# Optimization experiments

Hardware: AMD Instinct MI355X
Metric: run time of the kernel (lower is better)

Reference implementation:

```python
import jax, jax.numpy as jnp
import numpy as np

# Module constants from init_kwargs
A, T, HID, H, EGO = 50, 50, 128, 32, 0
C = 4 * HID // H   # per-head out channels = 16
B = 32
NEG_SLOPE = 0.2    # PyG GATConv default negative_slope


def setup_inputs() -> dict:
    key = jax.random.key(0)
    k1, k2, k3, k4 = jax.random.split(key, 4)
    h = jax.random.normal(k1, (B, A, T, HID), dtype=jnp.float32)
    # GATConv params: lin.weight (H*C, HID), att_src/att_dst (H, C), bias (H*C,)
    W = jax.random.normal(k2, (H * C, HID), dtype=jnp.float32) * (1.0 / np.sqrt(HID))
    att_src = jax.random.normal(k3, (H, C), dtype=jnp.float32) * 0.1
    att_dst = jax.random.normal(k4, (H, C), dtype=jnp.float32) * 0.1
    bias = jnp.zeros((H * C,), dtype=jnp.float32)
    return {"h": h, "W": W, "att_src": att_src, "att_dst": att_dst, "bias": bias}


def reference(h, W, att_src, att_dst, bias):
    # h: (B, A, T, HID). Node id = t*A + a after permute, matching build_ego_star_edges.
    b = h.shape[0]
    x = jnp.transpose(h, (0, 2, 1, 3))                       # (B, T, A, HID)
    # Linear projection into heads: (B, T, A, H, C)
    xw = jnp.einsum('btad,hcd->btahc', x, W.reshape(H, C, HID))
    a_src = jnp.einsum('btahc,hc->btah', xw, att_src)        # per-node src logit
    a_dst = jnp.einsum('btahc,hc->btah', xw, att_dst)        # per-node dst logit

    # Star topology: every (t_src, a != EGO) node -> every (t_dst, EGO) node.
    ne = jnp.array([a for a in range(A) if a != EGO])        # (A-1,) non-ego agents
    S = T * (A - 1)                                          # neighbors per ego dst
    x_ne = xw[:, :, ne].reshape(b, S, H, C)                  # (B, S, H, C)
    a_src_ne = a_src[:, :, ne].reshape(b, S, H)              # (B, S, H)
    a_dst_ego = a_dst[:, :, EGO]                             # (B, T, H)

    # Per-edge attention logits, segment-softmax over the S neighbors of each dst.
    logits = jax.nn.leaky_relu(a_src_ne[:, None, :, :] + a_dst_ego[:, :, None, :],
                               negative_slope=NEG_SLOPE)     # (B, T, S, H)
    att = jax.nn.softmax(logits, axis=2)

    # Weighted aggregation: (B, T, H, C) -> flatten heads (concat=True)
    out_ego = jnp.einsum('btsh,bshc->bthc', att, x_ne).reshape(b, T, H * C)

    # Nodes with no incoming edges get zero aggregation; bias added to all.
    out = jnp.zeros((b, T, A, H * C), dtype=h.dtype).at[:, :, EGO].set(out_ego)
    out = out + bias
    return jnp.transpose(out, (0, 2, 1, 3))                  # (B, A, T, H*C)
```

## Files before the change

### kernel.cpp

```cpp
#include <hip/hip_runtime.h>
#include <math.h>

#define NA    50
#define NT    50
#define HIDK  128
#define NH    32
#define NC    16
#define NB    32
#define SAT   2500
#define NS    2450
#define NOUT  512

__global__ __launch_bounds__(256) void k_fill(const float* __restrict__ bias,
                                              float* __restrict__ out) {
  size_t i = (size_t)blockIdx.x * 256 + threadIdx.x;
  float4 b4 = ((const float4*)bias)[i & 127];
  ((float4*)out)[i] = b4;
}

__global__ __launch_bounds__(256) void k0_pq(const float* __restrict__ W,
                                             const float* __restrict__ att_src,
                                             const float* __restrict__ att_dst,
                                             float* __restrict__ PQ) {
  int g = blockIdx.x * 256 + threadIdx.x;
  int j = g >> 7, k = g & 127;
  int hh = j & 31;
  const float* att = (j < 32) ? att_src : att_dst;
  float acc = 0.f;
  #pragma unroll
  for (int c = 0; c < 16; ++c)
    acc = fmaf(att[hh * 16 + c], W[(size_t)(hh * 16 + c) * 128 + k], acc);
  PQ[g] = acc;
}

__global__ __launch_bounds__(256) void k1_ud(
    const float* __restrict__ X,
    const float* __restrict__ PQ,
    float* __restrict__ u,
    float* __restrict__ dv)
{
  __shared__ float Ast[32][68];
  __shared__ float Bst[32][68];
  const int tid = threadIdx.x;
  const int m0 = blockIdx.x * 64;
  const int ty = tid >> 4, tx = tid & 15;
  float acc[4][4] = {};
  const int sr = tid >> 3, sc = tid & 7;

  for (int kc = 0; kc < 128; kc += 32) {
    #pragma unroll
    for (int L = 0; L < 2; ++L) {
      int row = sr + L * 32;
      float4 v = *(const float4*)&X[(size_t)(m0 + row) * 128 + kc + sc * 4];
      Ast[sc*4+0][row] = v.x; Ast[sc*4+1][row] = v.y;
      Ast[sc*4+2][row] = v.z; Ast[sc*4+3][row] = v.w;
      float4 w = *(const float4*)&PQ[(size_t)row * 128 + kc + sc * 4];
      Bst[sc*4+0][row] = w.x; Bst[sc*4+1][row] = w.y;
      Bst[sc*4+2][row] = w.z; Bst[sc*4+3][row] = w.w;
    }
    __syncthreads();
    #pragma unroll
    for (int k = 0; k < 32; ++k) {
      float4 a4 = *(const float4*)&Ast[k][ty * 4];
      float4 b4 = *(const float4*)&Bst[k][tx * 4];
      float a[4] = {a4.x, a4.y, a4.z, a4.w};
      float bb[4] = {b4.x, b4.y, b4.z, b4.w};
      #pragma unroll
      for (int i = 0; i < 4; ++i)
        #pragma unroll
        for (int j = 0; j < 4; ++j)
          acc[i][j] = fmaf(a[i], bb[j], acc[i][j]);
    }
    __syncthreads();
  }

  #pragma unroll
  for (int i = 0; i < 4; ++i) {
    int m = m0 + ty * 4 + i;
    int b = m / SAT, s = m - b * SAT;
    #pragma unroll
    for (int jj = 0; jj < 4; ++jj) {
      int col = tx * 4 + jj;
      if (col < 32)
        u[(size_t)(b * 32 + col) * SAT + s] = acc[i][jj];
      else if (s < NT)
        dv[(size_t)(b * 32 + col - 32) * NT + s] = acc[i][jj];
    }
  }
}

#define LOADG(B_, g_) do {                                                  \
    _Pragma("unroll")                                                       \
    for (int j = 0; j < 4; ++j) {                                           \
      int idx_ = base + 2 * ((g_) * 4 + j);                                 \
      e##B_[j] = sE[idx_]; s##B_[j] = sIdx[idx_];                           \
    }                                                                       \
    _Pragma("unroll")                                                       \
    for (int j = 0; j < 4; ++j)                                             \
      x##B_[j] = *(const float4*)(xb + (size_t)s##B_[j] * HIDK);            \
  } while (0)

#define COMPG(B_) do {                                                      \
    _Pragma("unroll")                                                       \
    for (int j = 0; j < 4; ++j) {                                           \
      float2 ee = e##B_[j]; float4 xx = x##B_[j];                           \
      a1[0]=fmaf(ee.x,xx.x,a1[0]); a1[1]=fmaf(ee.x,xx.y,a1[1]);             \
      a1[2]=fmaf(ee.x,xx.z,a1[2]); a1[3]=fmaf(ee.x,xx.w,a1[3]);             \
      a2[0]=fmaf(ee.y,xx.x,a2[0]); a2[1]=fmaf(ee.y,xx.y,a2[1]);             \
      a2[2]=fmaf(ee.y,xx.z,a2[2]); a2[3]=fmaf(ee.y,xx.w,a2[3]);             \
      z1 += ee.x; z2 += ee.y;                                               \
    }                                                                       \
  } while (0)

__global__ __launch_bounds__(512, 4) void k2_attn(
    const float* __restrict__ X,
    const float* __restrict__ u,
    const float* __restrict__ dv,
    const float* __restrict__ W,
    const float* __restrict__ bias,
    float* __restrict__ out)
{
  const int id = blockIdx.x;
  const int b  = (id & 7) + 8 * (id >> 8);
  const int h  = (id >> 3) & 31;
  const int tid = threadIdx.x;

  __shared__ float Bb[2][51][129];
  __shared__ float2 sE[NS];
  __shared__ unsigned short sIdx[NS];
  __shared__ float sTheta[50], sD[50], sF1[50], sF2[50];
  __shared__ int   sRank[50];
  __shared__ int   offs[52];
  __shared__ int   offCur[51];
  __shared__ float red[8];
  __shared__ float sMaxU;

  float* sU = &Bb[0][0][0];
  unsigned short* sBeta = (unsigned short*)&Bb[1][0][0];

  const size_t bh = (size_t)b * 32 + h;
  const float* uP = u + bh * SAT + NT;
  for (int i = tid; i < NS; i += 512) sU[i] = uP[i];
  if (tid < 50) sD[tid] = dv[bh * NT + tid];
  if (tid < 51) offCur[tid] = 0;
  __syncthreads();

  float mx = -1e30f;
  for (int i = tid; i < NS; i += 512) mx = fmaxf(mx, sU[i]);
  #pragma unroll
  for (int o = 32; o; o >>= 1) mx = fmaxf(mx, __shfl_xor(mx, o));
  if ((tid & 63) == 0) red[tid >> 6] = mx;
  __syncthreads();
  if (tid == 0) {
    float m2 = red[0];
    #pragma unroll
    for (int k = 1; k < 8; ++k) m2 = fmaxf(m2, red[k]);
    sMaxU = m2;
  }
  __syncthreads();
  const float maxU = sMaxU;

  if (tid < 50) {
    float th = -sD[tid];
    int r = 0;
    for (int t2 = 0; t2 < 50; ++t2) {
      float th2 = -sD[t2];
      r += (th2 < th) || (th2 == th && t2 < tid);
    }
    sRank[tid] = r;
    sTheta[r] = th;
    float x = maxU + sD[tid];
    float L = (x >= 0.f) ? x : 0.2f * x;
    sF1[tid] = __expf(x - L);
    sF2[tid] = __expf(0.2f * x - L);
  }
  __syncthreads();

  for (int i = tid; i < NS; i += 512) {
    float uu = sU[i];
    int lo = 0, hi = 50;
    while (lo < hi) { int mid = (lo + hi) >> 1; if (sTheta[mid] <= uu) lo = mid + 1; else hi = mid; }
    sBeta[i] = (unsigned short)lo;
    atomicAdd(&offCur[lo], 1);
  }
  __syncthreads();
  if (tid == 0) {
    int run = 0;
    for (int k = 0; k < 51; ++k) { int c = offCur[k]; offs[k] = run; run += c; }
    offs[51] = run;
  }
  __syncthreads();
  if (tid < 51) offCur[tid] = offs[tid];
  __syncthreads();

  for (int i = tid; i < NS; i += 512) {
    float uu = sU[i];
    int beta = sBeta[i];
    int pos = atomicAdd(&offCur[beta], 1);
    sE[pos] = make_float2(__expf(uu - maxU), __expf(0.2f * (uu - maxU)));
    sIdx[pos] = (unsigned short)(i + NT);
  }
  __syncthreads();

  {
    const int wave = tid >> 6;
    const int lane = tid & 63;
    const int slot = lane >> 5;
    const int cq   = lane & 31;
    const float* xb = X + (size_t)b * SAT * HIDK + cq * 4;

    for (int seg = wave; seg < 51; seg += 8) {
      const int i0 = offs[seg], i1 = offs[seg + 1];
      const int base = i0 + slot;
      int np = i1 - base;
      np = (np > 0) ? ((np + 1) >> 1) : 0;
      const int G = np >> 2;

      float a1[4] = {0.f, 0.f, 0.f, 0.f};
      float a2[4] = {0.f, 0.f, 0.f, 0.f};
      float z1 = 0.f, z2 = 0.f;

      float2 eA[4], eB[4]; int sA[4], sB[4]; float4 xA[4], xB[4];
      int g = 0;
      if (G) LOADG(A, 0);
      while (g + 2 <= G) {
        LOADG(B, g + 1);
        COMPG(A);
        if (g + 2 < G) LOADG(A, g + 2);
        COMPG(B);
        g += 2;
      }
      if (g < G) COMPG(A);
      for (int k = G * 4; k < np; ++k) {
        int idx = base + 2 * k;
        float2 ee = sE[idx];
        int ss = sIdx[idx];
        float4 xx = *(const float4*)(xb + (size_t)ss * HIDK);
        a1[0]=fmaf(ee.x,xx.x,a1[0]); a1[1]=fmaf(ee.x,xx.y,a1[1]);
        a1[2]=fmaf(ee.x,xx.z,a1[2]); a1[3]=fmaf(ee.x,xx.w,a1[3]);
        a2[0]=fmaf(ee.y,xx.x,a2[0]); a2[1]=fmaf(ee.y,xx.y,a2[1]);
        a2[2]=fmaf(ee.y,xx.z,a2[2]); a2[3]=fmaf(ee.y,xx.w,a2[3]);
        z1 += ee.x; z2 += ee.y;
      }

      #pragma unroll
      for (int j = 0; j < 4; ++j) {
        a1[j] += __shfl_xor(a1[j], 32);
        a2[j] += __shfl_xor(a2[j], 32);
      }
      z1 += __shfl_xor(z1, 32);
      z2 += __shfl_xor(z2, 32);
      if (slot == 0) {
        #pragma unroll
        for (int j = 0; j < 4; ++j) {
          Bb[0][seg][cq * 4 + j] = a1[j];
          Bb[1][seg][cq * 4 + j] = a2[j];
        }
        if (cq == 0) { Bb[0][seg][128] = z1; Bb[1][seg][128] = z2; }
      }
    }
  }
  __syncthreads();

  float* WshT = (float*)sE;
  const float* Wh = W + (size_t)h * 16 * 128;
  for (int v = tid; v < 2048; v += 512) {
    int k = v >> 4, cout = v & 15;
    WshT[k * 16 + cout] = Wh[(size_t)cout * 128 + k];
  }
  for (int task = tid; task < 258; task += 512) {
    int which = task >= 129;
    int c = task - which * 129;
    if (which == 0) {
      float run = 0.f;
      for (int k = 50; k >= 0; --k) { float tmp = Bb[0][k][c]; Bb[0][k][c] = run; run += tmp; }
    } else {
      float run = 0.f;
      for (int k = 0; k <= 50; ++k) { run += Bb[1][k][c]; Bb[1][k][c] = run; }
    }
  }
  __syncthreads();

  for (int task = tid; task < NT * NC; task += 512) {
    int t = task >> 4, cout = task & 15;
    int r = sRank[t];
    float F1 = sF1[t], F2 = sF2[t];
    float z = F1 * Bb[0][r][128] + F2 * Bb[1][r][128];
    const float* b1r = &Bb[0][r][0];
    const float* b2r = &Bb[1][r][0];
    float n1 = 0.f, n2 = 0.f;
    #pragma unroll 4
    for (int c = 0; c < 128; ++c) {
      float w = WshT[c * 16 + cout];
      n1 = fmaf(b1r[c], w, n1);
      n2 = fmaf(b2r[c], w, n2);
    }
    out[((size_t)b * SAT + t) * NOUT + h * 16 + cout] =
        (F1 * n1 + F2 * n2) / z + bias[h * 16 + cout];
  }
}

extern "C" void kernel_launch(void* const* d_in, const int* in_sizes, int n_in,
                              void* d_out, int out_size, void* d_ws, size_t ws_size,
                              hipStream_t stream) {
  const float* X       = (const float*)d_in[0];
  const float* Wm      = (const float*)d_in[1];
  const float* att_src = (const float*)d_in[2];
  const float* att_dst = (const float*)d_in[3];
  const float* bias    = (const float*)d_in[4];
  float* out = (float*)d_out;

  float* PQ = (float*)d_ws;
  float* u  = PQ + 64 * 128;
  float* dv = u + (size_t)NB * NH * SAT;

  hipLaunchKernelGGL(k_fill, dim3(40000), dim3(256), 0, stream, bias, out);
  hipLaunchKernelGGL(k0_pq, dim3(32), dim3(256), 0, stream, Wm, att_src, att_dst, PQ);
  hipLaunchKernelGGL(k1_ud, dim3(1250), dim3(256), 0, stream, X, PQ, u, dv);
  hipLaunchKernelGGL(k2_attn, dim3(1024), dim3(512), 0, stream,
                     X, u, dv, Wm, bias, out);
}
```

Baseline: 321.0 us.

## Split attention aggregation into four 32-channel passes, fold bias fill into k2

Restructures k2_attn so the weighted neighbor aggregation is done in four 32-channel passes. After each pass the partial sums are projected through a W slice and accumulated into a small 16-channel buffer, which shrinks shared memory enough to raise launch bounds to 8 blocks per CU. It stores only exp(0.2·x) per edge and recovers exp(x) as its fifth power. It fuses the max-reduction into the load, changes the batch-to-block mapping, and moves the non-ego bias fill into k2 so the separate k_fill launch is dropped. In exchange, X is read in four separate passes, each pass adds extra syncs, and the fifth-power trick may lose precision or underflow.

```diff
diff --git a/kernel.cpp b/kernel.cpp
--- a/kernel.cpp
+++ b/kernel.cpp
@@ -10,13 +10,6 @@
 #define SAT   2500
 #define NS    2450
 #define NOUT  512
-
-__global__ __launch_bounds__(256) void k_fill(const float* __restrict__ bias,
-                                              float* __restrict__ out) {
-  size_t i = (size_t)blockIdx.x * 256 + threadIdx.x;
-  float4 b4 = ((const float4*)bias)[i & 127];
-  ((float4*)out)[i] = b4;
-}
 
 __global__ __launch_bounds__(256) void k0_pq(const float* __restrict__ W,
                                              const float* __restrict__ att_src,
@@ -89,30 +82,54 @@
   }
 }
 
-#define LOADG(B_, g_) do {                                                  \
+
+#define OFF_BB     0
+#define OFF_SE2    13056
+#define OFF_SIDX   22856
+#define OFF_P      27756
+#define OFF_WT     34692
+#define OFF_THETA  36996
+#define OFF_SD     37196
+#define OFF_SF1    37396
+#define OFF_SF2    37596
+#define OFF_RANK   37796
+#define OFF_OFFS   37996
+#define OFF_OFFC   38204
+#define OFF_RED    38408
+#define OFF_MAXU   38440
+#define SMEM_BYTES 38448
+
+#define BB(s,k,c)  Bb[(((s)*51+(k))*32)+(c)]
+#define PP(s,k,c)  Pa[(((s)*51+(k))*17)+(c)]
+#define WT(co,c)   WshT[((co)*36)+(c)]
+
+#define LOADG2(B_, g_) do {                                                 \
     _Pragma("unroll")                                                       \
-    for (int j = 0; j < 4; ++j) {                                           \
-      int idx_ = base + 2 * ((g_) * 4 + j);                                 \
-      e##B_[j] = sE[idx_]; s##B_[j] = sIdx[idx_];                           \
+    for (int jj = 0; jj < 2; ++jj) {                                        \
+      int idx_ = j0 + 8 * (2 * (g_) + jj);                                  \
+      e##B_[jj] = sE2[idx_]; s##B_[jj] = sIdx[idx_];                        \
     }                                                                       \
     _Pragma("unroll")                                                       \
-    for (int j = 0; j < 4; ++j)                                             \
-      x##B_[j] = *(const float4*)(xb + (size_t)s##B_[j] * HIDK);            \
+    for (int jj = 0; jj < 2; ++jj)                                          \
+      x##B_[jj] = *(const float4*)(xb + (size_t)s##B_[jj] * HIDK);          \
   } while (0)
 
-#define COMPG(B_) do {                                                      \
+#define COMPG2(B_) do {                                                     \
     _Pragma("unroll")                                                       \
-    for (int j = 0; j < 4; ++j) {                                           \
-      float2 ee = e##B_[j]; float4 xx = x##B_[j];                           \
-      a1[0]=fmaf(ee.x,xx.x,a1[0]); a1[1]=fmaf(ee.x,xx.y,a1[1]);             \
-      a1[2]=fmaf(ee.x,xx.z,a1[2]); a1[3]=fmaf(ee.x,xx.w,a1[3]);             \
-      a2[0]=fmaf(ee.y,xx.x,a2[0]); a2[1]=fmaf(ee.y,xx.y,a2[1]);             \
-      a2[2]=fmaf(ee.y,xx.z,a2[2]); a2[3]=fmaf(ee.y,xx.w,a2[3]);             \
-      z1 += ee.x; z2 += ee.y;                                               \
+    for (int jj = 0; jj < 2; ++jj) {                                        \
+      float e2v = e##B_[jj];                                                \
+      float e2s = e2v * e2v;                                                \
+      float e1v = e2s * e2s * e2v;                                          \
+      float4 xx = x##B_[jj];                                                \
+      a1[0]=fmaf(e1v,xx.x,a1[0]); a1[1]=fmaf(e1v,xx.y,a1[1]);               \
+      a1[2]=fmaf(e1v,xx.z,a1[2]); a1[3]=fmaf(e1v,xx.w,a1[3]);               \
+      a2[0]=fmaf(e2v,xx.x,a2[0]); a2[1]=fmaf(e2v,xx.y,a2[1]);               \
+      a2[2]=fmaf(e2v,xx.z,a2[2]); a2[3]=fmaf(e2v,xx.w,a2[3]);               \
+      if (pass == 0) { z1 += e1v; z2 += e2v; }                              \
     }                                                                       \
   } while (0)
 
-__global__ __launch_bounds__(512, 4) void k2_attn(
+__global__ __launch_bounds__(512, 8) void k2_attn(
     const float* __restrict__ X,
     const float* __restrict__ u,
     const float* __restrict__ dv,
@@ -121,32 +138,35 @@
     float* __restrict__ out)
 {
   const int id = blockIdx.x;
-  const int b  = (id & 7) + 8 * (id >> 8);
+  const int b  = 4 * (id & 7) + (id >> 8);
   const int h  = (id >> 3) & 31;
   const int tid = threadIdx.x;
 
-  __shared__ float Bb[2][51][129];
-  __shared__ float2 sE[NS];
-  __shared__ unsigned short sIdx[NS];
-  __shared__ float sTheta[50], sD[50], sF1[50], sF2[50];
-  __shared__ int   sRank[50];
-  __shared__ int   offs[52];
-  __shared__ int   offCur[51];
-  __shared__ float red[8];
-  __shared__ float sMaxU;
-
-  float* sU = &Bb[0][0][0];
-  unsigned short* sBeta = (unsigned short*)&Bb[1][0][0];
+  __shared__ __align__(16) unsigned char smem[SMEM_BYTES];
+  float* Bb              = (float*)(smem + OFF_BB);
+  float* sE2             = (float*)(smem + OFF_SE2);
+  unsigned short* sIdx   = (unsigned short*)(smem + OFF_SIDX);
+  float* Pa              = (float*)(smem + OFF_P);
+  float* WshT            = (float*)(smem + OFF_WT);
+  float* sTheta          = (float*)(smem + OFF_THETA);
+  float* sD              = (float*)(smem + OFF_SD);
+  float* sF1             = (float*)(smem + OFF_SF1);
+  float* sF2             = (float*)(smem + OFF_SF2);
+  int*   sRank           = (int*)(smem + OFF_RANK);
+  int*   offs            = (int*)(smem + OFF_OFFS);
+  int*   offCur          = (int*)(smem + OFF_OFFC);
+  float* red             = (float*)(smem + OFF_RED);
+  float* sMaxU           = (float*)(smem + OFF_MAXU);
+  float* sU              = (float*)(smem + OFF_BB);
+  unsigned short* sBeta  = (unsigned short*)(smem + OFF_P);
 
   const size_t bh = (size_t)b * 32 + h;
   const float* uP = u + bh * SAT + NT;
-  for (int i = tid; i < NS; i += 512) sU[i] = uP[i];
+
+  float mx = -1e30f;
+  for (int i = tid; i < NS; i += 512) { float v = uP[i]; sU[i] = v; mx = fmaxf(mx, v); }
   if (tid < 50) sD[tid] = dv[bh * NT + tid];
   if (tid < 51) offCur[tid] = 0;
-  __syncthreads();
-
-  float mx = -1e30f;
-  for (int i = tid; i < NS; i += 512) mx = fmaxf(mx, sU[i]);
   #pragma unroll
   for (int o = 32; o; o >>= 1) mx = fmaxf(mx, __shfl_xor(mx, o));
   if ((tid & 63) == 0) red[tid >> 6] = mx;
@@ -155,10 +175,10 @@
     float m2 = red[0];
     #pragma unroll
     for (int k = 1; k < 8; ++k) m2 = fmaxf(m2, red[k]);
-    sMaxU = m2;
-  }
-  __syncthreads();
-  const float maxU = sMaxU;
+    sMaxU[0] = m2;
+  }
+  __syncthreads();
+  const float maxU = sMaxU[0];
 
   if (tid < 50) {
     float th = -sD[tid];
@@ -197,86 +217,106 @@
     float uu = sU[i];
     int beta = sBeta[i];
     int pos = atomicAdd(&offCur[beta], 1);
-    sE[pos] = make_float2(__expf(uu - maxU), __expf(0.2f * (uu - maxU)));
+    sE2[pos] = __expf(0.2f * (uu - maxU));
     sIdx[pos] = (unsigned short)(i + NT);
   }
   __syncthreads();
 
-  {
-    const int wave = tid >> 6;
-    const int lane = tid & 63;
-    const int slot = lane >> 5;
-    const int cq   = lane & 31;
-    const float* xb = X + (size_t)b * SAT * HIDK + cq * 4;
-
-    for (int seg = wave; seg < 51; seg += 8) {
-      const int i0 = offs[seg], i1 = offs[seg + 1];
-      const int base = i0 + slot;
-      int np = i1 - base;
-      np = (np > 0) ? ((np + 1) >> 1) : 0;
-      const int G = np >> 2;
-
-      float a1[4] = {0.f, 0.f, 0.f, 0.f};
-      float a2[4] = {0.f, 0.f, 0.f, 0.f};
-      float z1 = 0.f, z2 = 0.f;
-
-      float2 eA[4], eB[4]; int sA[4], sB[4]; float4 xA[4], xB[4];
-      int g = 0;
-      if (G) LOADG(A, 0);
-      while (g + 2 <= G) {
-        LOADG(B, g + 1);
-        COMPG(A);
-        if (g + 2 < G) LOADG(A, g + 2);
-        COMPG(B);
-        g += 2;
+  for (int i = tid; i < 1632; i += 512)
+    Pa[(i >> 4) * 17 + (i & 15)] = 0.f;
+
+  #pragma unroll
+  for (int pass = 0; pass < 4; ++pass) {
+    {
+      int cout = tid >> 5, k = tid & 31;
+      WT(cout, k) = W[(size_t)(h * 16 + cout) * 128 + pass * 32 + k];
+    }
+
+    {
+      const int wave = tid >> 6, lane = tid & 63;
+      const int slot = lane >> 3, cq = lane & 7;
+      const float* xb = X + (size_t)b * SAT * HIDK + pass * 32 + cq * 4;
+
+      for (int seg = wave; seg < 51; seg += 8) {
+        const int i0 = offs[seg], i1 = offs[seg + 1];
+        const int j0 = i0 + slot;
+        int d = i1 - j0;
+        int cnt = (d > 0) ? ((d + 7) >> 3) : 0;
+        int G = cnt >> 1;
+
+        float a1[4] = {0.f,0.f,0.f,0.f};
+        float a2[4] = {0.f,0.f,0.f,0.f};
+        float z1 = 0.f, z2 = 0.f;
+
+        float eA[2], eB[2]; int sA[2], sB[2]; float4 xA[2], xB[2];
+        int g = 0;
+        if (G) LOADG2(A, 0);
+        while (g + 2 <= G) {
+          LOADG2(B, g + 1);
+          COMPG2(A);
+          if (g + 2 < G) LOADG2(A, g + 2);
+          COMPG2(B);
+          g += 2;
+        }
+        if (g < G) COMPG2(A);
+        for (int kk = G * 2; kk < cnt; ++kk) {
+          int idx = j0 + 8 * kk;
+          float e2v = sE2[idx]; int ss = sIdx[idx];
+          float4 xx = *(const float4*)(xb + (size_t)ss * HIDK);
+          float e2s = e2v * e2v;
+          float e1v = e2s * e2s * e2v;
+          a1[0]=fmaf(e1v,xx.x,a1[0]); a1[1]=fmaf(e1v,xx.y,a1[1]);
+          a1[2]=fmaf(e1v,xx.z,a1[2]); a1[3]=fmaf(e1v,xx.w,a1[3]);
+          a2[0]=fmaf(e2v,xx.x,a2[0]); a2[1]=fmaf(e2v,xx.y,a2[1]);
+          a2[2]=fmaf(e2v,xx.z,a2[2]); a2[3]=fmaf(e2v,xx.w,a2[3]);
+          if (pass == 0) { z1 += e1v; z2 += e2v; }
+        }
+
+        #pragma unroll
+        for (int c = 0; c < 4; ++c) {
+          a1[c] += __shfl_xor(a1[c], 8);  a1[c] += __shfl_xor(a1[c], 16); a1[c] += __shfl_xor(a1[c], 32);
+          a2[c] += __shfl_xor(a2[c], 8);  a2[c] += __shfl_xor(a2[c], 16); a2[c] += __shfl_xor(a2[c], 32);
+        }
+        if (pass == 0) {
+          z1 += __shfl_xor(z1, 8); z1 += __shfl_xor(z1, 16); z1 += __shfl_xor(z1, 32);
+          z2 += __shfl_xor(z2, 8); z2 += __shfl_xor(z2, 16); z2 += __shfl_xor(z2, 32);
+        }
+        if (slot == 0) {
+          *(float4*)&BB(0, seg, cq * 4) = make_float4(a1[0], a1[1], a1[2], a1[3]);
+          *(float4*)&BB(1, seg, cq * 4) = make_float4(a2[0], a2[1], a2[2], a2[3]);
+          if (pass == 0 && lane == 0) { PP(0, seg, 16) = z1; PP(1, seg, 16) = z2; }
+        }
       }
-      if (g < G) COMPG(A);
-      for (int k = G * 4; k < np; ++k) {
-        int idx = base + 2 * k;
-        float2 ee = sE[idx];
-        int ss = sIdx[idx];
-        float4 xx = *(const float4*)(xb + (size_t)ss * HIDK);
-        a1[0]=fmaf(ee.x,xx.x,a1[0]); a1[1]=fmaf(ee.x,xx.y,a1[1]);
-        a1[2]=fmaf(ee.x,xx.z,a1[2]); a1[3]=fmaf(ee.x,xx.w,a1[3]);
-        a2[0]=fmaf(ee.y,xx.x,a2[0]); a2[1]=fmaf(ee.y,xx.y,a2[1]);
-        a2[2]=fmaf(ee.y,xx.z,a2[2]); a2[3]=fmaf(ee.y,xx.w,a2[3]);
-        z1 += ee.x; z2 += ee.y;
+    }
+    __syncthreads();
+
+    for (int t = tid; t < 1632; t += 512) {
+      int s = t >= 816;
+      int rkc = t - s * 816;
+      int k = rkc >> 4, cout = rkc & 15;
+      const float* br = &BB(s, k, 0);
+      const float* wr = &WT(cout, 0);
+      float acc = 0.f;
+      #pragma unroll
+      for (int c4 = 0; c4 < 8; ++c4) {
+        float4 bv = *(const float4*)(br + c4 * 4);
+        float4 wv = *(const float4*)(wr + c4 * 4);
+        acc = fmaf(bv.x, wv.x, fmaf(bv.y, wv.y, fmaf(bv.z, wv.z, fmaf(bv.w, wv.w, acc))));
       }
-
-      #pragma unroll
-      for (int j = 0; j < 4; ++j) {
-        a1[j] += __shfl_xor(a1[j], 32);
-        a2[j] += __shfl_xor(a2[j], 32);
-      }
-      z1 += __shfl_xor(z1, 32);
-      z2 += __shfl_xor(z2, 32);
-      if (slot == 0) {
-        #pragma unroll
-        for (int j = 0; j < 4; ++j) {
-          Bb[0][seg][cq * 4 + j] = a1[j];
-          Bb[1][seg][cq * 4 + j] = a2[j];
-        }
-        if (cq == 0) { Bb[0][seg][128] = z1; Bb[1][seg][128] = z2; }
-      }
-    }
-  }
-  __syncthreads();
-
-  float* WshT = (float*)sE;
-  const float* Wh = W + (size_t)h * 16 * 128;
-  for (int v = tid; v < 2048; v += 512) {
-    int k = v >> 4, cout = v & 15;
-    WshT[k * 16 + cout] = Wh[(size_t)cout * 128 + k];
-  }
-  for (int task = tid; task < 258; task += 512) {
-    int which = task >= 129;
-    int c = task - which * 129;
-    if (which == 0) {
+      PP(s, k, cout) += acc;
+    }
+    __syncthreads();
+  }
+
+  if (tid < 34) {
+    int s = tid >= 17;
+    int cout = tid - s * 17;
+    if (s == 0) {
       float run = 0.f;
-      for (int k = 50; k >= 0; --k) { float tmp = Bb[0][k][c]; Bb[0][k][c] = run; run += tmp; }
+      for (int k = 50; k >= 0; --k) { float tmp = PP(0, k, cout); PP(0, k, cout) = run; run += tmp; }
     } else {
       float run = 0.f;
-      for (int k = 0; k <= 50; ++k) { run += Bb[1][k][c]; Bb[1][k][c] = run; }
+      for (int k = 0; k <= 50; ++k) { run += PP(1, k, cout); PP(1, k, cout) = run; }
     }
   }
   __syncthreads();
@@ -285,18 +325,21 @@
     int t = task >> 4, cout = task & 15;
     int r = sRank[t];
     float F1 = sF1[t], F2 = sF2[t];
-    float z = F1 * Bb[0][r][128] + F2 * Bb[1][r][128];
-    const float* b1r = &Bb[0][r][0];
-    const float* b2r = &Bb[1][r][0];
-    float n1 = 0.f, n2 = 0.f;
-    #pragma unroll 4
-    for (int c = 0; c < 128; ++c) {
-      float w = WshT[c * 16 + cout];
-      n1 = fmaf(b1r[c], w, n1);
-      n2 = fmaf(b2r[c], w, n2);
-    }
-    out[((size_t)b * SAT + t) * NOUT + h * 16 + cout] =
-        (F1 * n1 + F2 * n2) / z + bias[h * 16 + cout];
+    float z = F1 * PP(0, r, 16) + F2 * PP(1, r, 16);
+    float n = F1 * PP(0, r, cout) + F2 * PP(1, r, cout);
+    out[((size_t)b * SAT + t) * NOUT + h * 16 + cout] = n / z + bias[h * 16 + cout];
+  }
+
+  {
+    int g0 = id * 9800 + tid;
+    const float4 b4 = ((const float4*)bias)[g0 & 127];
+    float4* o4 = (float4*)out;
+    int gEnd = (id + 1) * 9800;
+    for (int g = g0; g < gEnd; g += 512) {
+      int bb2 = g / 313600;
+      int o = g - bb2 * 313600;
+      o4[(size_t)bb2 * 320000 + 6400 + o] = b4;
+    }
   }
 }
 
@@ -314,7 +357,6 @@
   float* u  = PQ + 64 * 128;
   float* dv = u + (size_t)NB * NH * SAT;
 
-  hipLaunchKernelGGL(k_fill, dim3(40000), dim3(256), 0, stream, bias, out);
   hipLaunchKernelGGL(k0_pq, dim3(32), dim3(256), 0, stream, Wm, att_src, att_dst, PQ);
   hipLaunchKernelGGL(k1_ud, dim3(1250), dim3(256), 0, stream, X, PQ, u, dv);
   hipLaunchKernelGGL(k2_attn, dim3(1024), dim3(512), 0, stream,
```

Result: slower. 407.7 us (+27.0%).
